# Optimization experiments

Measured on AMD Instinct MI355X. Metric: run time of the kernel, lower is better.

## Reference

```python
import jax, jax.numpy as jnp
import numpy as np

N_NODES = 50000
D_FEAT = 512
H1, H2 = 128, 64
N_CLASSES = 40
E_MP = 800000
E_LP = 250000


def gcn_conv(x, W, b, edge_index, edge_weight, num_nodes):
    """PyG GCNConv: add self-loops, symmetric norm D^-1/2 (A+I) D^-1/2, then (norm-agg)(xW)+b."""
    row, col = edge_index[0], edge_index[1]
    loop = jnp.arange(num_nodes)
    row = jnp.concatenate([row, loop])
    col = jnp.concatenate([col, loop])
    ew = jnp.concatenate([edge_weight, jnp.ones((num_nodes,), x.dtype)])
    deg = jax.ops.segment_sum(ew, col, num_segments=num_nodes)
    dinv = jnp.where(deg > 0, deg ** -0.5, 0.0).astype(x.dtype)
    norm = dinv[row] * ew * dinv[col]  # [E+N]
    h = x @ W  # [N, out]
    msg = h[row] * norm[:, None]  # gather + scale per edge
    out = jax.ops.segment_sum(msg, col, num_segments=num_nodes) + b
    return out


def setup_inputs() -> dict:
    key = jax.random.key(0)
    ks = jax.random.split(key, 16)
    inp = {}
    inp["x"] = jax.random.normal(ks[0], (N_NODES, D_FEAT), jnp.float32)
    inp["train_pos_edge_index"] = jax.random.randint(ks[1], (2, E_MP), 0, N_NODES)
    inp["edge_index"] = jax.random.randint(ks[2], (2, E_MP), 0, N_NODES)
    inp["edge_weight"] = jax.random.uniform(ks[3], (E_MP,), jnp.float32)
    inp["pos_edge_index"] = jax.random.randint(ks[4], (2, E_LP), 0, N_NODES)
    inp["neg_edge_index"] = jax.random.randint(ks[5], (2, E_LP), 0, N_NODES)
    # parameters (glorot-ish scaled)
    def w(k, i, o):
        return jax.random.normal(k, (i, o), jnp.float32) * (2.0 / (i + o)) ** 0.5
    inp["W1"] = w(ks[6], D_FEAT, H1)
    inp["b1"] = jnp.zeros((H1,), jnp.float32)
    inp["W2"] = w(ks[7], H1, H2)
    inp["b2"] = jnp.zeros((H2,), jnp.float32)
    inp["W_attr"] = w(ks[8], H2, N_CLASSES)
    inp["b_attr"] = jnp.zeros((N_CLASSES,), jnp.float32)
    inp["W_att"] = w(ks[9], H2, N_CLASSES)
    inp["b_att"] = jnp.zeros((N_CLASSES,), jnp.float32)
    return inp


def reference(x, train_pos_edge_index, edge_index, edge_weight, pos_edge_index,
              neg_edge_index, W1, b1, W2, b2, W_attr, b_attr, W_att, b_att):
    ones = jnp.ones((train_pos_edge_index.shape[1],), x.dtype)
    h = jax.nn.relu(gcn_conv(x, W1, b1, train_pos_edge_index, ones, N_NODES))
    h = gcn_conv(h, W2, b2, train_pos_edge_index, ones, N_NODES)  # [N, 64]
    attr = gcn_conv(h, W_attr, b_attr, edge_index, edge_weight, N_NODES)
    # gradient reversal is identity in forward
    att = gcn_conv(h, W_att, b_att, edge_index, edge_weight, N_NODES)
    total = jnp.concatenate([pos_edge_index, neg_edge_index], axis=-1)  # [2, 2*E_LP]
    x_j = h[total[0]]
    x_i = h[total[1]]
    res = jnp.einsum("ef,ef->e", x_i, x_j)
    return res, jax.nn.log_softmax(attr, axis=1), jax.nn.log_softmax(att, axis=1)
```

## Files before the change

kernel.cpp:

```cpp
#include <hip/hip_runtime.h>

typedef short s16x8 __attribute__((ext_vector_type(8)));
typedef float f32x4 __attribute__((ext_vector_type(4)));

static __device__ __forceinline__ unsigned short f2bf(float f) {
  unsigned u = __float_as_uint(f);
  u += 0x7fff + ((u >> 16) & 1);
  return (unsigned short)(u >> 16);
}
static __device__ __forceinline__ float bf2f(unsigned short h) {
  return __uint_as_float(((unsigned)h) << 16);
}


static __global__ void k_init(int* cntT, int* cntE, int n) {
  int i = blockIdx.x * blockDim.x + threadIdx.x;
  if (i < n) { cntT[i] = 0; cntE[i] = 0; }
}

static __global__ void k_count(const int* __restrict__ tcol, const int* __restrict__ ecol,
                               int* __restrict__ cntT, int* __restrict__ cntE,
                               int* __restrict__ rankT, int* __restrict__ rankE, int E) {
  int base = (blockIdx.x * blockDim.x + threadIdx.x) * 4;
  if (base + 3 < E) {
    int4 tc = *(const int4*)&tcol[base];
    int4 ec = *(const int4*)&ecol[base];
    int4 rt, re;
    rt.x = atomicAdd(&cntT[tc.x], 1);
    rt.y = atomicAdd(&cntT[tc.y], 1);
    rt.z = atomicAdd(&cntT[tc.z], 1);
    rt.w = atomicAdd(&cntT[tc.w], 1);
    re.x = atomicAdd(&cntE[ec.x], 1);
    re.y = atomicAdd(&cntE[ec.y], 1);
    re.z = atomicAdd(&cntE[ec.z], 1);
    re.w = atomicAdd(&cntE[ec.w], 1);
    *(int4*)&rankT[base] = rt;
    *(int4*)&rankE[base] = re;
  } else {
    for (int e = base; e < E; ++e) {
      rankT[e] = atomicAdd(&cntT[tcol[e]], 1);
      rankE[e] = atomicAdd(&cntE[ecol[e]], 1);
    }
  }
}

static __global__ __launch_bounds__(256) void k_scanA(
    const int* __restrict__ cntT, const int* __restrict__ cntE,
    int* __restrict__ bsum, int n, int nb) {
  const int* cnt = blockIdx.y ? cntE : cntT;
  int tid = threadIdx.x;
  int base = blockIdx.x * 1024 + tid * 4;
  int s = 0;
#pragma unroll
  for (int q = 0; q < 4; ++q) { int i = base + q; if (i < n) s += cnt[i]; }
  __shared__ int red[256];
  red[tid] = s;
  __syncthreads();
  for (int off = 128; off > 0; off >>= 1) {
    if (tid < off) red[tid] += red[tid + off];
    __syncthreads();
  }
  if (tid == 0) bsum[blockIdx.y * nb + blockIdx.x] = red[0];
}

static __global__ void k_scanB(int* bsum, int* ptrT, int* ptrE, int nb, int n) {
  int a = threadIdx.x;
  if (a > 1) return;
  int* bs = bsum + a * nb;
  int run = 0;
  for (int i = 0; i < nb; ++i) { int c = bs[i]; bs[i] = run; run += c; }
  (a ? ptrE : ptrT)[n] = run;
}

static __global__ __launch_bounds__(256) void k_scanC(
    const int* __restrict__ cntT, const int* __restrict__ cntE,
    const int* __restrict__ bsum, int* __restrict__ ptrT, int* __restrict__ ptrE,
    int n, int nb) {
  const int* cnt = blockIdx.y ? cntE : cntT;
  int* ptr = blockIdx.y ? ptrE : ptrT;
  int tid = threadIdx.x;
  int pre = bsum[blockIdx.y * nb + blockIdx.x];
  int base = blockIdx.x * 1024 + tid * 4;
  int v[4];
  int s = 0;
#pragma unroll
  for (int q = 0; q < 4; ++q) { int i = base + q; v[q] = (i < n) ? cnt[i] : 0; s += v[q]; }
  __shared__ int red[256];
  red[tid] = s;
  __syncthreads();
  for (int off = 1; off < 256; off <<= 1) {
    int t = (tid >= off) ? red[tid - off] : 0;
    __syncthreads();
    red[tid] += t;
    __syncthreads();
  }
  int run = pre + (tid ? red[tid - 1] : 0);
#pragma unroll
  for (int q = 0; q < 4; ++q) {
    int i = base + q;
    if (i < n) ptr[i] = run;
    run += v[q];
  }
}

static __global__ void k_fill(const int* __restrict__ trow, const int* __restrict__ tcol,
                              const int* __restrict__ erow, const int* __restrict__ ecol,
                              const float* __restrict__ ew,
                              const int* __restrict__ ptrT, const int* __restrict__ ptrE,
                              const int* __restrict__ rankT, const int* __restrict__ rankE,
                              int* __restrict__ srcT, int2* __restrict__ srcwE, int E) {
  int base = (blockIdx.x * blockDim.x + threadIdx.x) * 4;
  if (base + 3 < E) {
    int4 tr = *(const int4*)&trow[base];
    int4 tc = *(const int4*)&tcol[base];
    int4 er = *(const int4*)&erow[base];
    int4 ec = *(const int4*)&ecol[base];
    float4 w = *(const float4*)&ew[base];
    int4 rt = *(const int4*)&rankT[base];
    int4 re = *(const int4*)&rankE[base];
    srcT[ptrT[tc.x] + rt.x] = tr.x;
    srcT[ptrT[tc.y] + rt.y] = tr.y;
    srcT[ptrT[tc.z] + rt.z] = tr.z;
    srcT[ptrT[tc.w] + rt.w] = tr.w;
    int2 p;
    p.x = er.x; p.y = __float_as_int(w.x); srcwE[ptrE[ec.x] + re.x] = p;
    p.x = er.y; p.y = __float_as_int(w.y); srcwE[ptrE[ec.y] + re.y] = p;
    p.x = er.z; p.y = __float_as_int(w.z); srcwE[ptrE[ec.z] + re.z] = p;
    p.x = er.w; p.y = __float_as_int(w.w); srcwE[ptrE[ec.w] + re.w] = p;
  } else {
    for (int e = base; e < E; ++e) {
      srcT[ptrT[tcol[e]] + rankT[e]] = trow[e];
      int2 p;
      p.x = erow[e];
      p.y = __float_as_int(ew[e]);
      srcwE[ptrE[ecol[e]] + rankE[e]] = p;
    }
  }
}

static __global__ void k_dinv2(const int* __restrict__ cntT, const int2* __restrict__ srcwE,
                               const int* __restrict__ ptrE,
                               float* __restrict__ dinvT, float* __restrict__ dinvE, int n) {
  int i = blockIdx.x * blockDim.x + threadIdx.x;
  if (i >= n) return;
  dinvT[i] = rsqrtf((float)cntT[i] + 1.0f);
  float s = 1.0f;
  int e = ptrE[i + 1];
  for (int j = ptrE[i]; j < e; ++j) s += __int_as_float(srcwE[j].y);
  dinvE[i] = rsqrtf(s);
}


static __global__ void k_cvtW(const float* __restrict__ W, unsigned short* __restrict__ Wh,
                              unsigned short* __restrict__ Wl, int K, int Nc) {
  int t = blockIdx.x * blockDim.x + threadIdx.x;
  if (t >= K * Nc) return;
  int k = t / Nc, c = t - k * Nc;
  float v = W[t];
  unsigned short hi = f2bf(v);
  size_t o = (size_t)(k >> 5) * (Nc * 32) + c * 32 + (k & 31);
  Wh[o] = hi;
  Wl[o] = f2bf(v - bf2f(hi));
}


#define GK 512
#define NKT 16

static __device__ __forceinline__ void cvt8(float4 a, float4 b, s16x8& hi, s16x8& lo) {
  float f[8] = {a.x, a.y, a.z, a.w, b.x, b.y, b.z, b.w};
#pragma unroll
  for (int i = 0; i < 8; ++i) {
    unsigned short h = f2bf(f[i]);
    hi[i] = (short)h;
    lo[i] = (short)f2bf(f[i] - bf2f(h));
  }
}

static __global__ __launch_bounds__(256, 2) void k_gemm_mfma_split(
    const float* __restrict__ A, const unsigned short* __restrict__ Bh,
    const unsigned short* __restrict__ Bl, float* __restrict__ C, int M) {
  int tid = threadIdx.x;
  int lane = tid & 63, wid = tid >> 6;
  int wr = wid >> 1, wc = wid & 1;
  int l15 = lane & 15, l4 = lane >> 4;
  int brow = blockIdx.x * 64;
  f32x4 acc[2][4] = {};

  const float* arow[2];
#pragma unroll
  for (int m = 0; m < 2; ++m) {
    int r = brow + wr * 32 + m * 16 + l15;
    arow[m] = &A[(size_t)min(r, M - 1) * GK + l4 * 8];
  }
  size_t boff = (size_t)(wc * 64 + l15) * 32 + l4 * 8;

#pragma unroll
  for (int kt = 0; kt < NKT; ++kt) {
    s16x8 afh[2], afl[2];
#pragma unroll
    for (int m = 0; m < 2; ++m) {
      float4 a0 = *(const float4*)(arow[m] + kt * 32);
      float4 a1 = *(const float4*)(arow[m] + kt * 32 + 4);
      cvt8(a0, a1, afh[m], afl[m]);
    }
    s16x8 bh[4], bl[4];
#pragma unroll
    for (int n = 0; n < 4; ++n) {
      size_t o = (size_t)kt * 4096 + boff + n * 512;
      bh[n] = *(const s16x8*)&Bh[o];
      bl[n] = *(const s16x8*)&Bl[o];
    }
#pragma unroll
    for (int m = 0; m < 2; ++m)
#pragma unroll
      for (int n = 0; n < 4; ++n) {
        acc[m][n] = __builtin_amdgcn_mfma_f32_16x16x32_bf16(afh[m], bh[n], acc[m][n], 0, 0, 0);
        acc[m][n] = __builtin_amdgcn_mfma_f32_16x16x32_bf16(afl[m], bh[n], acc[m][n], 0, 0, 0);
        acc[m][n] = __builtin_amdgcn_mfma_f32_16x16x32_bf16(afh[m], bl[n], acc[m][n], 0, 0, 0);
      }
  }

#pragma unroll
  for (int m = 0; m < 2; ++m) {
    int rbase = brow + wr * 32 + m * 16 + l4 * 4;
#pragma unroll
    for (int n = 0; n < 4; ++n) {
      int c = wc * 64 + n * 16 + l15;
#pragma unroll
      for (int j = 0; j < 4; ++j) {
        int r = rbase + j;
        if (r < M) C[(size_t)r * 128 + c] = acc[m][n][j];
      }
    }
  }
}


template <int F, bool RELU, bool WEIGHTED>
static __global__ __launch_bounds__(256) void k_gather4(
    const float* __restrict__ H, const int* __restrict__ rowptr,
    const int* __restrict__ src, const int2* __restrict__ srcw,
    const float* __restrict__ dinv, const float* __restrict__ Hpre,
    const float* __restrict__ bias, float* __restrict__ out, int n) {
  const int L = F / 4;
  int node = blockIdx.x * (256 / L) + threadIdx.x / L;
  if (node >= n) return;
  int f4 = (threadIdx.x % L) * 4;
  float d = dinv[node];
  float4 hp = *(const float4*)&Hpre[(size_t)node * F + f4];
  float ax = hp.x * d, ay = hp.y * d, az = hp.z * d, aw = hp.w * d;
  int j = rowptr[node], e = rowptr[node + 1];
  for (; j + 1 < e; j += 2) {
    int r0, r1;
    float w0, w1;
    if (WEIGHTED) {
      int2 a = srcw[j], b = srcw[j + 1];
      r0 = a.x; r1 = b.x;
      w0 = dinv[r0] * __int_as_float(a.y);
      w1 = dinv[r1] * __int_as_float(b.y);
    } else {
      r0 = src[j]; r1 = src[j + 1];
      w0 = dinv[r0]; w1 = dinv[r1];
    }
    float4 v0 = *(const float4*)&H[(size_t)r0 * F + f4];
    float4 v1 = *(const float4*)&H[(size_t)r1 * F + f4];
    ax += v0.x * w0 + v1.x * w1;
    ay += v0.y * w0 + v1.y * w1;
    az += v0.z * w0 + v1.z * w1;
    aw += v0.w * w0 + v1.w * w1;
  }
  if (j < e) {
    int r;
    float wj;
    if (WEIGHTED) { int2 a = srcw[j]; r = a.x; wj = dinv[r] * __int_as_float(a.y); }
    else { r = src[j]; wj = dinv[r]; }
    float4 v = *(const float4*)&H[(size_t)r * F + f4];
    ax += v.x * wj; ay += v.y * wj; az += v.z * wj; aw += v.w * wj;
  }
  float bx = 0, by = 0, bz = 0, bw = 0;
  if (bias) { float4 bb = *(const float4*)&bias[f4]; bx = bb.x; by = bb.y; bz = bb.z; bw = bb.w; }
  ax = ax * d + bx; ay = ay * d + by; az = az * d + bz; aw = aw * d + bw;
  if (RELU) { ax = fmaxf(ax, 0.f); ay = fmaxf(ay, 0.f); az = fmaxf(az, 0.f); aw = fmaxf(aw, 0.f); }
  float4 o; o.x = ax; o.y = ay; o.z = az; o.w = aw;
  *(float4*)&out[(size_t)node * F + f4] = o;
}


static __global__ __launch_bounds__(256) void k_gemm(
    const float* __restrict__ A, const float* __restrict__ B,
    const float* __restrict__ bias, float* __restrict__ C,
    int M, int N, int K) {
  const int BM = 64, BN = 64, BK = 16;
  __shared__ float As[BK][BM + 4];
  __shared__ float Bs[BK][BN + 4];
  int tid = threadIdx.x;
  int tr = tid >> 4, tc = tid & 15;
  int brow = blockIdx.y * BM, bcol = blockIdx.x * BN;
  float acc[4][4] = {};
  for (int k0 = 0; k0 < K; k0 += BK) {
#pragma unroll
    for (int i = tid; i < BM * BK; i += 256) {
      int m = i >> 4, kk = i & 15;
      int gr = brow + m;
      As[kk][m] = (gr < M) ? A[(size_t)gr * K + k0 + kk] : 0.f;
    }
#pragma unroll
    for (int i = tid; i < BK * BN; i += 256) {
      int kk = i >> 6, n = i & 63;
      int gc = bcol + n;
      Bs[kk][n] = (gc < N) ? B[(size_t)(k0 + kk) * N + gc] : 0.f;
    }
    __syncthreads();
#pragma unroll
    for (int kk = 0; kk < BK; ++kk) {
      float a[4], b[4];
#pragma unroll
      for (int i = 0; i < 4; ++i) a[i] = As[kk][tr * 4 + i];
#pragma unroll
      for (int j = 0; j < 4; ++j) b[j] = Bs[kk][tc * 4 + j];
#pragma unroll
      for (int i = 0; i < 4; ++i)
#pragma unroll
        for (int j = 0; j < 4; ++j) acc[i][j] += a[i] * b[j];
    }
    __syncthreads();
  }
#pragma unroll
  for (int i = 0; i < 4; ++i) {
    int r = brow + tr * 4 + i;
    if (r >= M) continue;
#pragma unroll
    for (int j = 0; j < 4; ++j) {
      int c = bcol + tc * 4 + j;
      if (c < N) C[(size_t)r * N + c] = acc[i][j] + (bias ? bias[c] : 0.f);
    }
  }
}


static __global__ void k_logsoftmax40(float* __restrict__ X, int n) {
  int i = blockIdx.x * blockDim.x + threadIdx.x;
  if (i >= n) return;
  float4 v[10];
#pragma unroll
  for (int q = 0; q < 10; ++q) v[q] = *(const float4*)&X[(size_t)i * 40 + q * 4];
  float m = -1e30f;
#pragma unroll
  for (int q = 0; q < 10; ++q)
    m = fmaxf(m, fmaxf(fmaxf(v[q].x, v[q].y), fmaxf(v[q].z, v[q].w)));
  float s = 0.f;
#pragma unroll
  for (int q = 0; q < 10; ++q)
    s += expf(v[q].x - m) + expf(v[q].y - m) + expf(v[q].z - m) + expf(v[q].w - m);
  float ls = logf(s) + m;
#pragma unroll
  for (int q = 0; q < 10; ++q) {
    float4 o; o.x = v[q].x - ls; o.y = v[q].y - ls; o.z = v[q].z - ls; o.w = v[q].w - ls;
    *(float4*)&X[(size_t)i * 40 + q * 4] = o;
  }
}


static __global__ __launch_bounds__(256) void k_linkpred4(
    const float* __restrict__ H2, const int* __restrict__ pos,
    const int* __restrict__ neg, float* __restrict__ res, int Elp) {
  int t = blockIdx.x * 256 + threadIdx.x;
  int e = t >> 4, f4 = (t & 15) * 4;
  if (e >= 2 * Elp) return;
  int a, b;
  if (e < Elp) { a = pos[e]; b = pos[Elp + e]; }
  else { int e2 = e - Elp; a = neg[e2]; b = neg[Elp + e2]; }
  float4 va = *(const float4*)&H2[(size_t)a * 64 + f4];
  float4 vb = *(const float4*)&H2[(size_t)b * 64 + f4];
  float p = va.x * vb.x + va.y * vb.y + va.z * vb.z + va.w * vb.w;
  p += __shfl_xor(p, 1);
  p += __shfl_xor(p, 2);
  p += __shfl_xor(p, 4);
  p += __shfl_xor(p, 8);
  if ((t & 15) == 0) res[e] = p;
}


extern "C" void kernel_launch(void* const* d_in, const int* in_sizes, int n_in,
                              void* d_out, int out_size, void* d_ws, size_t ws_size,
                              hipStream_t stream) {
  const float* x    = (const float*)d_in[0];
  const int*   tp   = (const int*)d_in[1];
  const int*   ei   = (const int*)d_in[2];
  const float* ew   = (const float*)d_in[3];
  const int*   pos  = (const int*)d_in[4];
  const int*   neg  = (const int*)d_in[5];
  const float* W1   = (const float*)d_in[6];
  const float* b1   = (const float*)d_in[7];
  const float* W2   = (const float*)d_in[8];
  const float* b2   = (const float*)d_in[9];
  const float* Wattr= (const float*)d_in[10];
  const float* battr= (const float*)d_in[11];
  const float* Watt = (const float*)d_in[12];
  const float* batt = (const float*)d_in[13];

  const int N   = in_sizes[0] / 512;
  const int EMP = in_sizes[1] / 2;
  const int ELP = in_sizes[4] / 2;
  const int NB  = (N + 1023) / 1024;

  float* ws = (float*)d_ws;
  float* dinvT = ws;
  float* dinvE = dinvT + N;
  int* rowptrT = (int*)(dinvE + N);
  int* rowptrE = rowptrT + (N + 4);
  int* srcT    = rowptrE + (N + 4);
  int2* srcwE  = (int2*)(srcT + EMP);
  int* bsum    = (int*)(srcwE + EMP);
  unsigned short* W1h = (unsigned short*)(bsum + 128);
  unsigned short* W1l = W1h + 512 * 128;
  float* bufA  = (float*)(W1l + 512 * 128);
  float* bufB  = bufA + (size_t)N * 128;
  float* bufC  = bufB + (size_t)N * 128;
  int* rankT = (int*)bufA;
  int* rankE = rankT + EMP;
  int* cntT  = (int*)bufB;
  int* cntE  = cntT + N;

  float* out_res  = (float*)d_out;
  float* out_attr = out_res + 2 * (size_t)ELP;
  float* out_att  = out_attr + (size_t)N * 40;

  dim3 b256(256);
  int gN = (N + 255) / 256;
  int gE4 = (EMP + 1023) / 1024;

  k_init<<<gN, b256, 0, stream>>>(cntT, cntE, N);
  k_cvtW<<<(512 * 128 + 255) / 256, b256, 0, stream>>>(W1, W1h, W1l, 512, 128);
  k_count<<<gE4, b256, 0, stream>>>(tp + EMP, ei + EMP, cntT, cntE, rankT, rankE, EMP);
  {
    dim3 gs(NB, 2);
    k_scanA<<<gs, b256, 0, stream>>>(cntT, cntE, bsum, N, NB);
    k_scanB<<<1, 64, 0, stream>>>(bsum, rowptrT, rowptrE, NB, N);
    k_scanC<<<gs, b256, 0, stream>>>(cntT, cntE, bsum, rowptrT, rowptrE, N, NB);
  }
  k_fill<<<gE4, b256, 0, stream>>>(tp, tp + EMP, ei, ei + EMP, ew,
                                   rowptrT, rowptrE, rankT, rankE, srcT, srcwE, EMP);
  k_dinv2<<<gN, b256, 0, stream>>>(cntT, srcwE, rowptrE, dinvT, dinvE, N);

  k_gemm_mfma_split<<<(N + 63) / 64, b256, 0, stream>>>(x, W1h, W1l, bufA, N);
  k_gather4<128, true, false><<<(N + 7) / 8, b256, 0, stream>>>(
      bufA, rowptrT, srcT, nullptr, dinvT, bufA, b1, bufB, N);

  {
    dim3 grid(1, (N + 63) / 64);
    k_gemm<<<grid, b256, 0, stream>>>(bufB, W2, nullptr, bufA, N, 64, 128);
  }
  k_gather4<64, false, false><<<(N + 15) / 16, b256, 0, stream>>>(
      bufA, rowptrT, srcT, nullptr, dinvT, bufA, b2, bufC, N);

  k_gather4<64, false, true><<<(N + 15) / 16, b256, 0, stream>>>(
      bufC, rowptrE, nullptr, srcwE, dinvE, bufC, nullptr, bufA, N);

  {
    dim3 grid(1, (N + 63) / 64);
    k_gemm<<<grid, b256, 0, stream>>>(bufA, Wattr, battr, out_attr, N, 40, 64);
    k_gemm<<<grid, b256, 0, stream>>>(bufA, Watt, batt, out_att, N, 40, 64);
  }
  k_logsoftmax40<<<gN, b256, 0, stream>>>(out_attr, N);
  k_logsoftmax40<<<gN, b256, 0, stream>>>(out_att, N);

  k_linkpred4<<<(2 * ELP * 16 + 255) / 256, b256, 0, stream>>>(bufC, pos, neg, out_res, ELP);
}
```

Baseline: 454.8 us.

## Double-buffer A and B register prefetch in split-bf16 MFMA GEMM

Adds a two-stage register prefetch in the x@W1 MFMA GEMM. A and B fragments for tile kt+2 are loaded while tile kt is converted and multiplied, and a sched_barrier keeps the A loads ahead of the MFMA block. Launch bounds are raised from 2 to 3 waves per SIMD to increase occupancy. This should hide global load latency, at the cost of more live registers, which under the tighter register cap could cause spills.

```diff
diff --git a/kernel.cpp b/kernel.cpp
--- a/kernel.cpp
+++ b/kernel.cpp
@@ -177,7 +177,7 @@
   }
 }
 
-static __global__ __launch_bounds__(256, 2) void k_gemm_mfma_split(
+static __global__ __launch_bounds__(256, 3) void k_gemm_mfma_split(
     const float* __restrict__ A, const unsigned short* __restrict__ Bh,
     const unsigned short* __restrict__ Bl, float* __restrict__ C, int M) {
   int tid = threadIdx.x;
@@ -195,30 +195,56 @@
   }
   size_t boff = (size_t)(wc * 64 + l15) * 32 + l4 * 8;
 
+  float4 aP[2][2][2];
+  s16x8 bhP[2][4], blP[2][4];
+
+#pragma unroll
+  for (int s = 0; s < 2; ++s)
+#pragma unroll
+    for (int m = 0; m < 2; ++m) {
+      aP[s][m][0] = *(const float4*)(arow[m] + s * 32);
+      aP[s][m][1] = *(const float4*)(arow[m] + s * 32 + 4);
+    }
+#pragma unroll
+  for (int s = 0; s < 2; ++s)
+#pragma unroll
+    for (int n = 0; n < 4; ++n) {
+      size_t o = (size_t)s * 4096 + boff + n * 512;
+      bhP[s][n] = *(const s16x8*)&Bh[o];
+      blP[s][n] = *(const s16x8*)&Bl[o];
+    }
+
 #pragma unroll
   for (int kt = 0; kt < NKT; ++kt) {
+    const int S = kt & 1;
     s16x8 afh[2], afl[2];
 #pragma unroll
-    for (int m = 0; m < 2; ++m) {
-      float4 a0 = *(const float4*)(arow[m] + kt * 32);
-      float4 a1 = *(const float4*)(arow[m] + kt * 32 + 4);
-      cvt8(a0, a1, afh[m], afl[m]);
-    }
-    s16x8 bh[4], bl[4];
-#pragma unroll
-    for (int n = 0; n < 4; ++n) {
-      size_t o = (size_t)kt * 4096 + boff + n * 512;
-      bh[n] = *(const s16x8*)&Bh[o];
-      bl[n] = *(const s16x8*)&Bl[o];
-    }
-#pragma unroll
     for (int m = 0; m < 2; ++m)
+      cvt8(aP[S][m][0], aP[S][m][1], afh[m], afl[m]);
+    if (kt + 2 < NKT) {
+#pragma unroll
+      for (int m = 0; m < 2; ++m) {
+        aP[S][m][0] = *(const float4*)(arow[m] + (kt + 2) * 32);
+        aP[S][m][1] = *(const float4*)(arow[m] + (kt + 2) * 32 + 4);
+      }
+    }
+    __builtin_amdgcn_sched_barrier(0);
+#pragma unroll
+    for (int m = 0; m < 2; ++m)
 #pragma unroll
       for (int n = 0; n < 4; ++n) {
-        acc[m][n] = __builtin_amdgcn_mfma_f32_16x16x32_bf16(afh[m], bh[n], acc[m][n], 0, 0, 0);
-        acc[m][n] = __builtin_amdgcn_mfma_f32_16x16x32_bf16(afl[m], bh[n], acc[m][n], 0, 0, 0);
-        acc[m][n] = __builtin_amdgcn_mfma_f32_16x16x32_bf16(afh[m], bl[n], acc[m][n], 0, 0, 0);
+        acc[m][n] = __builtin_amdgcn_mfma_f32_16x16x32_bf16(afh[m], bhP[S][n], acc[m][n], 0, 0, 0);
+        acc[m][n] = __builtin_amdgcn_mfma_f32_16x16x32_bf16(afl[m], bhP[S][n], acc[m][n], 0, 0, 0);
+        acc[m][n] = __builtin_amdgcn_mfma_f32_16x16x32_bf16(afh[m], blP[S][n], acc[m][n], 0, 0, 0);
       }
+    if (kt + 2 < NKT) {
+      size_t o = (size_t)(kt + 2) * 4096 + boff;
+#pragma unroll
+      for (int n = 0; n < 4; ++n) {
+        bhP[S][n] = *(const s16x8*)&Bh[o + n * 512];
+        blP[S][n] = *(const s16x8*)&Bl[o + n * 512];
+      }
+    }
   }
 
 #pragma unroll
```

Measured after the change: 452.7 us. Within noise of the previous version (-0.5%).

## Fold source normalization into CSR entries and fuse both heads with log-softmax

Applied to the files above, without the earlier changes.

The weighted degree is now accumulated with float atomics during counting, so dinv can be computed before the fill. The fill kernel then stores the premultiplied source weight (dinv[row]*ew) alongside the row index for both graphs. This removes the per-edge dinv gather from every aggregation pass and drops the serial per-node degree loop. The two 40-class head GEMMs and both log-softmax launches are replaced by one shared-memory kernel that computes both heads and normalizes in place, cutting launches and global round trips. The trade-offs are float atomics, which make the degree sums order-nondeterministic, and a larger int2 CSR for the unweighted graph.

```diff
diff --git a/kernel.cpp b/kernel.cpp
--- a/kernel.cpp
+++ b/kernel.cpp
@@ -13,18 +13,21 @@
 }
 
 
-static __global__ void k_init(int* cntT, int* cntE, int n) {
+static __global__ void k_init(int* cntT, int* cntE, float* degE, int n) {
   int i = blockIdx.x * blockDim.x + threadIdx.x;
-  if (i < n) { cntT[i] = 0; cntE[i] = 0; }
+  if (i < n) { cntT[i] = 0; cntE[i] = 0; degE[i] = 1.0f; }
 }
 
 static __global__ void k_count(const int* __restrict__ tcol, const int* __restrict__ ecol,
+                               const float* __restrict__ ew,
                                int* __restrict__ cntT, int* __restrict__ cntE,
+                               float* __restrict__ degE,
                                int* __restrict__ rankT, int* __restrict__ rankE, int E) {
   int base = (blockIdx.x * blockDim.x + threadIdx.x) * 4;
   if (base + 3 < E) {
     int4 tc = *(const int4*)&tcol[base];
     int4 ec = *(const int4*)&ecol[base];
+    float4 w = *(const float4*)&ew[base];
     int4 rt, re;
     rt.x = atomicAdd(&cntT[tc.x], 1);
     rt.y = atomicAdd(&cntT[tc.y], 1);
@@ -34,12 +37,17 @@
     re.y = atomicAdd(&cntE[ec.y], 1);
     re.z = atomicAdd(&cntE[ec.z], 1);
     re.w = atomicAdd(&cntE[ec.w], 1);
+    atomicAdd(&degE[ec.x], w.x);
+    atomicAdd(&degE[ec.y], w.y);
+    atomicAdd(&degE[ec.z], w.z);
+    atomicAdd(&degE[ec.w], w.w);
     *(int4*)&rankT[base] = rt;
     *(int4*)&rankE[base] = re;
   } else {
     for (int e = base; e < E; ++e) {
       rankT[e] = atomicAdd(&cntT[tcol[e]], 1);
       rankE[e] = atomicAdd(&cntE[ecol[e]], 1);
+      atomicAdd(&degE[ecol[e]], ew[e]);
     }
   }
 }
@@ -103,12 +111,21 @@
   }
 }
 
+static __global__ void k_dinv(const int* __restrict__ cntT, const float* __restrict__ degE,
+                              float* __restrict__ dinvT, float* __restrict__ dinvE, int n) {
+  int i = blockIdx.x * blockDim.x + threadIdx.x;
+  if (i >= n) return;
+  dinvT[i] = rsqrtf((float)cntT[i] + 1.0f);
+  dinvE[i] = rsqrtf(degE[i]);
+}
+
 static __global__ void k_fill(const int* __restrict__ trow, const int* __restrict__ tcol,
                               const int* __restrict__ erow, const int* __restrict__ ecol,
                               const float* __restrict__ ew,
+                              const float* __restrict__ dinvT, const float* __restrict__ dinvE,
                               const int* __restrict__ ptrT, const int* __restrict__ ptrE,
                               const int* __restrict__ rankT, const int* __restrict__ rankE,
-                              int* __restrict__ srcT, int2* __restrict__ srcwE, int E) {
+                              int2* __restrict__ srcwT, int2* __restrict__ srcwE, int E) {
   int base = (blockIdx.x * blockDim.x + threadIdx.x) * 4;
   if (base + 3 < E) {
     int4 tr = *(const int4*)&trow[base];
@@ -118,36 +135,24 @@
     float4 w = *(const float4*)&ew[base];
     int4 rt = *(const int4*)&rankT[base];
     int4 re = *(const int4*)&rankE[base];
-    srcT[ptrT[tc.x] + rt.x] = tr.x;
-    srcT[ptrT[tc.y] + rt.y] = tr.y;
-    srcT[ptrT[tc.z] + rt.z] = tr.z;
-    srcT[ptrT[tc.w] + rt.w] = tr.w;
     int2 p;
-    p.x = er.x; p.y = __float_as_int(w.x); srcwE[ptrE[ec.x] + re.x] = p;
-    p.x = er.y; p.y = __float_as_int(w.y); srcwE[ptrE[ec.y] + re.y] = p;
-    p.x = er.z; p.y = __float_as_int(w.z); srcwE[ptrE[ec.z] + re.z] = p;
-    p.x = er.w; p.y = __float_as_int(w.w); srcwE[ptrE[ec.w] + re.w] = p;
+    p.x = tr.x; p.y = __float_as_int(dinvT[tr.x]); srcwT[ptrT[tc.x] + rt.x] = p;
+    p.x = tr.y; p.y = __float_as_int(dinvT[tr.y]); srcwT[ptrT[tc.y] + rt.y] = p;
+    p.x = tr.z; p.y = __float_as_int(dinvT[tr.z]); srcwT[ptrT[tc.z] + rt.z] = p;
+    p.x = tr.w; p.y = __float_as_int(dinvT[tr.w]); srcwT[ptrT[tc.w] + rt.w] = p;
+    p.x = er.x; p.y = __float_as_int(dinvE[er.x] * w.x); srcwE[ptrE[ec.x] + re.x] = p;
+    p.x = er.y; p.y = __float_as_int(dinvE[er.y] * w.y); srcwE[ptrE[ec.y] + re.y] = p;
+    p.x = er.z; p.y = __float_as_int(dinvE[er.z] * w.z); srcwE[ptrE[ec.z] + re.z] = p;
+    p.x = er.w; p.y = __float_as_int(dinvE[er.w] * w.w); srcwE[ptrE[ec.w] + re.w] = p;
   } else {
     for (int e = base; e < E; ++e) {
-      srcT[ptrT[tcol[e]] + rankT[e]] = trow[e];
       int2 p;
-      p.x = erow[e];
-      p.y = __float_as_int(ew[e]);
+      p.x = trow[e]; p.y = __float_as_int(dinvT[trow[e]]);
+      srcwT[ptrT[tcol[e]] + rankT[e]] = p;
+      p.x = erow[e]; p.y = __float_as_int(dinvE[erow[e]] * ew[e]);
       srcwE[ptrE[ecol[e]] + rankE[e]] = p;
     }
   }
-}
-
-static __global__ void k_dinv2(const int* __restrict__ cntT, const int2* __restrict__ srcwE,
-                               const int* __restrict__ ptrE,
-                               float* __restrict__ dinvT, float* __restrict__ dinvE, int n) {
-  int i = blockIdx.x * blockDim.x + threadIdx.x;
-  if (i >= n) return;
-  dinvT[i] = rsqrtf((float)cntT[i] + 1.0f);
-  float s = 1.0f;
-  int e = ptrE[i + 1];
-  for (int j = ptrE[i]; j < e; ++j) s += __int_as_float(srcwE[j].y);
-  dinvE[i] = rsqrtf(s);
 }
 
 
@@ -237,12 +242,12 @@
 }
 
 
-template <int F, bool RELU, bool WEIGHTED>
+template <int F, bool RELU>
 static __global__ __launch_bounds__(256) void k_gather4(
     const float* __restrict__ H, const int* __restrict__ rowptr,
-    const int* __restrict__ src, const int2* __restrict__ srcw,
-    const float* __restrict__ dinv, const float* __restrict__ Hpre,
-    const float* __restrict__ bias, float* __restrict__ out, int n) {
+    const int2* __restrict__ srcw, const float* __restrict__ dinv,
+    const float* __restrict__ Hpre, const float* __restrict__ bias,
+    float* __restrict__ out, int n) {
   const int L = F / 4;
   int node = blockIdx.x * (256 / L) + threadIdx.x / L;
   if (node >= n) return;
@@ -252,30 +257,20 @@
   float ax = hp.x * d, ay = hp.y * d, az = hp.z * d, aw = hp.w * d;
   int j = rowptr[node], e = rowptr[node + 1];
   for (; j + 1 < e; j += 2) {
-    int r0, r1;
-    float w0, w1;
-    if (WEIGHTED) {
-      int2 a = srcw[j], b = srcw[j + 1];
-      r0 = a.x; r1 = b.x;
-      w0 = dinv[r0] * __int_as_float(a.y);
-      w1 = dinv[r1] * __int_as_float(b.y);
-    } else {
-      r0 = src[j]; r1 = src[j + 1];
-      w0 = dinv[r0]; w1 = dinv[r1];
-    }
-    float4 v0 = *(const float4*)&H[(size_t)r0 * F + f4];
-    float4 v1 = *(const float4*)&H[(size_t)r1 * F + f4];
+    int2 a = srcw[j], b = srcw[j + 1];
+    float w0 = __int_as_float(a.y);
+    float w1 = __int_as_float(b.y);
+    float4 v0 = *(const float4*)&H[(size_t)a.x * F + f4];
+    float4 v1 = *(const float4*)&H[(size_t)b.x * F + f4];
     ax += v0.x * w0 + v1.x * w1;
     ay += v0.y * w0 + v1.y * w1;
     az += v0.z * w0 + v1.z * w1;
     aw += v0.w * w0 + v1.w * w1;
   }
   if (j < e) {
-    int r;
-    float wj;
-    if (WEIGHTED) { int2 a = srcw[j]; r = a.x; wj = dinv[r] * __int_as_float(a.y); }
-    else { r = src[j]; wj = dinv[r]; }
-    float4 v = *(const float4*)&H[(size_t)r * F + f4];
+    int2 a = srcw[j];
+    float wj = __int_as_float(a.y);
+    float4 v = *(const float4*)&H[(size_t)a.x * F + f4];
     ax += v.x * wj; ay += v.y * wj; az += v.z * wj; aw += v.w * wj;
   }
   float bx = 0, by = 0, bz = 0, bw = 0;
@@ -339,25 +334,54 @@
 }
 
 
-static __global__ void k_logsoftmax40(float* __restrict__ X, int n) {
-  int i = blockIdx.x * blockDim.x + threadIdx.x;
-  if (i >= n) return;
-  float4 v[10];
-#pragma unroll
-  for (int q = 0; q < 10; ++q) v[q] = *(const float4*)&X[(size_t)i * 40 + q * 4];
-  float m = -1e30f;
-#pragma unroll
-  for (int q = 0; q < 10; ++q)
-    m = fmaxf(m, fmaxf(fmaxf(v[q].x, v[q].y), fmaxf(v[q].z, v[q].w)));
-  float s = 0.f;
-#pragma unroll
-  for (int q = 0; q < 10; ++q)
-    s += expf(v[q].x - m) + expf(v[q].y - m) + expf(v[q].z - m) + expf(v[q].w - m);
-  float ls = logf(s) + m;
-#pragma unroll
-  for (int q = 0; q < 10; ++q) {
-    float4 o; o.x = v[q].x - ls; o.y = v[q].y - ls; o.z = v[q].z - ls; o.w = v[q].w - ls;
-    *(float4*)&X[(size_t)i * 40 + q * 4] = o;
+static __global__ __launch_bounds__(256) void k_heads(
+    const float* __restrict__ H, const float* __restrict__ Wattr,
+    const float* __restrict__ battr, const float* __restrict__ Watt,
+    const float* __restrict__ batt, float* __restrict__ out_attr,
+    float* __restrict__ out_att, int n) {
+  __shared__ float Hs[64][65];
+  __shared__ float Ws[64][80];
+  __shared__ float bs[80];
+  __shared__ float Os[64][82];
+  int tid = threadIdx.x;
+  int node0 = blockIdx.x * 64;
+  for (int i = tid; i < 1024; i += 256) {
+    int r = i >> 4, c4 = (i & 15) * 4;
+    float4 v = (node0 + r < n) ? *(const float4*)&H[(size_t)(node0 + r) * 64 + c4]
+                               : make_float4(0.f, 0.f, 0.f, 0.f);
+    Hs[r][c4] = v.x; Hs[r][c4 + 1] = v.y; Hs[r][c4 + 2] = v.z; Hs[r][c4 + 3] = v.w;
+  }
+  for (int i = tid; i < 64 * 40; i += 256) {
+    int k = i / 40, j = i - k * 40;
+    Ws[k][j] = Wattr[i];
+    Ws[k][40 + j] = Watt[i];
+  }
+  if (tid < 40) { bs[tid] = battr[tid]; bs[40 + tid] = batt[tid]; }
+  __syncthreads();
+
+  int r = tid & 63, g = tid >> 6;
+  float acc[20];
+#pragma unroll
+  for (int j = 0; j < 20; ++j) acc[j] = bs[g * 20 + j];
+  for (int k = 0; k < 64; ++k) {
+    float h = Hs[r][k];
+#pragma unroll
+    for (int j = 0; j < 20; ++j) acc[j] += h * Ws[k][g * 20 + j];
+  }
+#pragma unroll
+  for (int j = 0; j < 20; ++j) Os[r][g * 20 + j] = acc[j];
+  __syncthreads();
+
+  if (tid < 128 && node0 + (tid & 63) < n) {
+    int r2 = tid & 63;
+    int base = (tid >> 6) * 40;
+    float m = -1e30f;
+    for (int j = 0; j < 40; ++j) m = fmaxf(m, Os[r2][base + j]);
+    float s = 0.f;
+    for (int j = 0; j < 40; ++j) s += expf(Os[r2][base + j] - m);
+    float ls = logf(s) + m;
+    float* o = (tid < 64 ? out_attr : out_att) + (size_t)(node0 + r2) * 40;
+    for (int j = 0; j < 40; ++j) o[j] = Os[r2][base + j] - ls;
   }
 }
 
@@ -410,8 +434,8 @@
   float* dinvE = dinvT + N;
   int* rowptrT = (int*)(dinvE + N);
   int* rowptrE = rowptrT + (N + 4);
-  int* srcT    = rowptrE + (N + 4);
-  int2* srcwE  = (int2*)(srcT + EMP);
+  int2* srcwT  = (int2*)(rowptrE + (N + 4));
+  int2* srcwE  = srcwT + EMP;
   int* bsum    = (int*)(srcwE + EMP);
   unsigned short* W1h = (unsigned short*)(bsum + 128);
   unsigned short* W1l = W1h + 512 * 128;
@@ -420,8 +444,9 @@
   float* bufC  = bufB + (size_t)N * 128;
   int* rankT = (int*)bufA;
   int* rankE = rankT + EMP;
-  int* cntT  = (int*)bufB;
-  int* cntE  = cntT + N;
+  int*   cntT = (int*)bufB;
+  int*   cntE = cntT + N;
+  float* degE = (float*)(cntE + N);
 
   float* out_res  = (float*)d_out;
   float* out_attr = out_res + 2 * (size_t)ELP;
@@ -431,40 +456,36 @@
   int gN = (N + 255) / 256;
   int gE4 = (EMP + 1023) / 1024;
 
-  k_init<<<gN, b256, 0, stream>>>(cntT, cntE, N);
+  k_init<<<gN, b256, 0, stream>>>(cntT, cntE, degE, N);
   k_cvtW<<<(512 * 128 + 255) / 256, b256, 0, stream>>>(W1, W1h, W1l, 512, 128);
-  k_count<<<gE4, b256, 0, stream>>>(tp + EMP, ei + EMP, cntT, cntE, rankT, rankE, EMP);
+  k_count<<<gE4, b256, 0, stream>>>(tp + EMP, ei + EMP, ew, cntT, cntE, degE,
+                                    rankT, rankE, EMP);
   {
     dim3 gs(NB, 2);
     k_scanA<<<gs, b256, 0, stream>>>(cntT, cntE, bsum, N, NB);
     k_scanB<<<1, 64, 0, stream>>>(bsum, rowptrT, rowptrE, NB, N);
     k_scanC<<<gs, b256, 0, stream>>>(cntT, cntE, bsum, rowptrT, rowptrE, N, NB);
   }
-  k_fill<<<gE4, b256, 0, stream>>>(tp, tp + EMP, ei, ei + EMP, ew,
-                                   rowptrT, rowptrE, rankT, rankE, srcT, srcwE, EMP);
-  k_dinv2<<<gN, b256, 0, stream>>>(cntT, srcwE, rowptrE, dinvT, dinvE, N);
+  k_dinv<<<gN, b256, 0, stream>>>(cntT, degE, dinvT, dinvE, N);
+  k_fill<<<gE4, b256, 0, stream>>>(tp, tp + EMP, ei, ei + EMP, ew, dinvT, dinvE,
+                                   rowptrT, rowptrE, rankT, rankE, srcwT, srcwE, EMP);
 
   k_gemm_mfma_split<<<(N + 63) / 64, b256, 0, stream>>>(x, W1h, W1l, bufA, N);
-  k_gather4<128, true, false><<<(N + 7) / 8, b256, 0, stream>>>(
-      bufA, rowptrT, srcT, nullptr, dinvT, bufA, b1, bufB, N);
+  k_gather4<128, true><<<(N + 7) / 8, b256, 0, stream>>>(
+      bufA, rowptrT, srcwT, dinvT, bufA, b1, bufB, N);
 
   {
     dim3 grid(1, (N + 63) / 64);
     k_gemm<<<grid, b256, 0, stream>>>(bufB, W2, nullptr, bufA, N, 64, 128);
   }
-  k_gather4<64, false, false><<<(N + 15) / 16, b256, 0, stream>>>(
-      bufA, rowptrT, srcT, nullptr, dinvT, bufA, b2, bufC, N);
-
-  k_gather4<64, false, true><<<(N + 15) / 16, b256, 0, stream>>>(
-      bufC, rowptrE, nullptr, srcwE, dinvE, bufC, nullptr, bufA, N);
-
-  {
-    dim3 grid(1, (N + 63) / 64);
-    k_gemm<<<grid, b256, 0, stream>>>(bufA, Wattr, battr, out_attr, N, 40, 64);
-    k_gemm<<<grid, b256, 0, stream>>>(bufA, Watt, batt, out_att, N, 40, 64);
-  }
-  k_logsoftmax40<<<gN, b256, 0, stream>>>(out_attr, N);
-  k_logsoftmax40<<<gN, b256, 0, stream>>>(out_att, N);
+  k_gather4<64, false><<<(N + 15) / 16, b256, 0, stream>>>(
+      bufA, rowptrT, srcwT, dinvT, bufA, b2, bufC, N);
+
+  k_gather4<64, false><<<(N + 15) / 16, b256, 0, stream>>>(
+      bufC, rowptrE, srcwE, dinvE, bufC, nullptr, bufA, N);
+
+  k_heads<<<(N + 63) / 64, b256, 0, stream>>>(
+      bufA, Wattr, battr, Watt, batt, out_attr, out_att, N);
 
   k_linkpred4<<<(2 * ELP * 16 + 255) / 256, b256, 0, stream>>>(bufC, pos, neg, out_res, ELP);
 }
```

After: 495.5 us. 1.09x slower.
